# Optimization experiments

Measured on AMD Instinct MI355X. Metric: run time of the kernel, lower is better.

The kernel has to match this reference:

```python
import jax, jax.numpy as jnp
import numpy as np

MAX_TOTAL = 20        # max_total_size
MAX_PER_CLASS = 20    # max_output_size_per_class
SCORE_TH = 0.5        # score_threshold
IOU_TH = 0.5          # tf combined NMS default iou_threshold
K_CAND = 200          # top candidates per class considered for NMS
VARIANCES = jnp.array([0.1, 0.1, 0.2, 0.2], jnp.float32)


def setup_inputs() -> dict:
    key = jax.random.key(0)
    k1, k2, k3, k4, k5, k6 = jax.random.split(key, 6)
    B, N, C = 64, 8732, 21
    pred_deltas = jax.random.normal(k1, (B, N, 4), jnp.float32)
    pred_labels = jax.random.uniform(k2, (B, N, C), dtype=jnp.float32)
    # synthetic normalized anchors (y1,x1,y2,x2) with valid extents
    cy = jax.random.uniform(k3, (N,), dtype=jnp.float32)
    cx = jax.random.uniform(k4, (N,), dtype=jnp.float32)
    h = jax.random.uniform(k5, (N,), dtype=jnp.float32, minval=0.05, maxval=0.3)
    w = jax.random.uniform(k6, (N,), dtype=jnp.float32, minval=0.05, maxval=0.3)
    anchors = jnp.stack([cy - h / 2, cx - w / 2, cy + h / 2, cx + w / 2], axis=-1)
    return {"pred_deltas": pred_deltas, "pred_labels": pred_labels, "anchors": anchors}


def _decode(anchors, deltas):
    # anchors [N,4] (y1,x1,y2,x2); deltas [B,N,4] (dy,dx,dh,dw) -> boxes [B,N,4]
    ah = anchors[:, 2] - anchors[:, 0]
    aw = anchors[:, 3] - anchors[:, 1]
    acy = anchors[:, 0] + 0.5 * ah
    acx = anchors[:, 1] + 0.5 * aw
    cy = deltas[..., 0] * ah + acy
    cx = deltas[..., 1] * aw + acx
    h = jnp.exp(deltas[..., 2]) * ah
    w = jnp.exp(deltas[..., 3]) * aw
    return jnp.stack([cy - 0.5 * h, cx - 0.5 * w, cy + 0.5 * h, cx + 0.5 * w], axis=-1)


def _pairwise_iou(boxes):
    # boxes [K,4] -> iou [K,K]
    y1, x1, y2, x2 = boxes[:, 0], boxes[:, 1], boxes[:, 2], boxes[:, 3]
    area = (y2 - y1) * (x2 - x1)
    ih = jnp.clip(jnp.minimum(y2[:, None], y2[None, :]) - jnp.maximum(y1[:, None], y1[None, :]), 0.0)
    iw = jnp.clip(jnp.minimum(x2[:, None], x2[None, :]) - jnp.maximum(x1[:, None], x1[None, :]), 0.0)
    inter = ih * iw
    return inter / (area[:, None] + area[None, :] - inter + 1e-8)


def _nms_one_class(scores, boxes):
    # scores [N], boxes [N,4] -> (top scores [MAX_PER_CLASS], boxes [MAX_PER_CLASS,4])
    vals, idx = jax.lax.top_k(scores, K_CAND)          # sorted desc
    cboxes = boxes[idx]                                # [K,4]
    iou = _pairwise_iou(cboxes)                        # [K,K]
    valid = vals > SCORE_TH
    ar = jnp.arange(K_CAND)

    def body(i, keep):
        suppressed = jnp.any(keep & (iou[i] > IOU_TH) & (ar < i))
        return keep.at[i].set(valid[i] & ~suppressed)

    keep = jax.lax.fori_loop(0, K_CAND, body, jnp.zeros(K_CAND, dtype=bool))
    kept_scores = jnp.where(keep, vals, 0.0)
    top_vals, top_i = jax.lax.top_k(kept_scores, MAX_PER_CLASS)
    return top_vals, cboxes[top_i]


def reference(pred_deltas, pred_labels, anchors):
    deltas = pred_deltas * VARIANCES                       # variance scaling
    boxes = _decode(anchors, deltas)                       # [B,N,4]
    # zero out all class scores where argmax class == 0 (background)
    lab_map = jnp.argmax(pred_labels, axis=-1, keepdims=True)
    scores = jnp.where(lab_map != 0, pred_labels, 0.0)     # [B,N,C]

    per_class = jax.vmap(_nms_one_class, in_axes=(1, None))   # over classes
    per_batch = jax.vmap(per_class, in_axes=(0, 0))           # over batch
    cls_scores, cls_boxes = per_batch(scores, boxes)          # [B,C,P], [B,C,P,4]

    B, C, P = cls_scores.shape
    flat_scores = cls_scores.reshape(B, C * P)
    flat_boxes = cls_boxes.reshape(B, C * P, 4)
    class_ids = jnp.broadcast_to(jnp.arange(C, dtype=jnp.float32)[:, None], (C, P)).reshape(-1)

    top_vals, top_i = jax.lax.top_k(flat_scores, MAX_TOTAL)   # [B,MAX_TOTAL]
    final_boxes = jnp.take_along_axis(flat_boxes, top_i[..., None], axis=1)
    final_boxes = jnp.clip(final_boxes, 0.0, 1.0)             # combined NMS clip_boxes=True
    valid = top_vals > 0.0
    final_boxes = jnp.where(valid[..., None], final_boxes, 0.0)
    final_labels = jnp.where(valid, class_ids[top_i], 0.0)
    return final_boxes, top_vals, final_labels
```

## Files before the change

### kernel.cpp

```cpp
#include <hip/hip_runtime.h>
#include <stdint.h>

typedef unsigned long long u64;
typedef unsigned int u32;

#define BATCH 64
#define NANCH 8732
#define NF4   2183
#define NCLS 21
#define KCAND 200
#define PPC 20
#define PTOT 20

__global__ __launch_bounds__(256) void kdecode(
    const float* __restrict__ deltas, const float* __restrict__ labels,
    const float* __restrict__ anchors, float* __restrict__ boxes,
    unsigned char* __restrict__ msk, float* __restrict__ scoresT, int useT)
{
#pragma clang fp contract(off)
    int n = blockIdx.x * 256 + threadIdx.x;
    int b = blockIdx.y;
    if (n >= NANCH) return;
    const float* lab = labels + ((size_t)b * NANCH + n) * NCLS;
    float v[NCLS];
#pragma unroll
    for (int c = 0; c < NCLS; ++c) v[c] = lab[c];
    float mx = v[0]; int am = 0;
#pragma unroll
    for (int c = 1; c < NCLS; ++c) if (v[c] > mx) { mx = v[c]; am = c; }
    bool mk = (am != 0);
    msk[(size_t)b * NANCH + n] = mk ? 1 : 0;
    if (useT) {
#pragma unroll
        for (int c = 0; c < NCLS; ++c)
            scoresT[((size_t)b * NCLS + c) * NANCH + n] = mk ? v[c] : 0.0f;
    }
    float4 d = ((const float4*)deltas)[(size_t)b * NANCH + n];
    float4 a = ((const float4*)anchors)[n];
    float ah = a.z - a.x, aw = a.w - a.y;
    float acy = a.x + 0.5f * ah, acx = a.y + 0.5f * aw;
    float cy = (d.x * 0.1f) * ah + acy;
    float cx = (d.y * 0.1f) * aw + acx;
    float hh = expf(d.z * 0.2f) * ah;
    float ww = expf(d.w * 0.2f) * aw;
    float4 o;
    o.x = cy - 0.5f * hh; o.y = cx - 0.5f * ww;
    o.z = cy + 0.5f * hh; o.w = cx + 0.5f * ww;
    ((float4*)boxes)[(size_t)b * NANCH + n] = o;
}

__device__ __forceinline__ u64 shflxor64(u64 x, int m) {
    return (u64)__shfl_xor((long long)x, m, 64);
}

__device__ __forceinline__ void suffixFind(const u32* hist, u32* waveTot, int nb, int need,
                                           int* sSel, int* sAbove, int* sH,
                                           int tid, int lane, int wv)
{
    int K = (nb + 255) >> 8;
    int base = tid * K;
    u32 own = 0;
    for (int q = 0; q < K; ++q) { int bi = base + q; own += (bi < nb) ? hist[bi] : 0u; }
    u32 s = own;
#pragma unroll
    for (int d = 1; d < 64; d <<= 1) {
        u32 o = __shfl_down(s, d, 64);
        if (lane + d < 64) s += o;
    }
    if (lane == 0) waveTot[wv] = s;
    __syncthreads();
    u32 add = 0;
    for (int w = wv + 1; w < 4; ++w) add += waveTot[w];
    u32 cum = (s - own) + add;
    for (int q = K - 1; q >= 0; --q) {
        int bi = base + q;
        u32 hh = (bi < nb) ? hist[bi] : 0u;
        if (cum < (u32)need && cum + hh >= (u32)need) { *sSel = bi; *sAbove = (int)cum; *sH = (int)hh; }
        cum += hh;
    }
    __syncthreads();
}

__global__ __launch_bounds__(256) void knms(
    const float* __restrict__ labels, const unsigned char* __restrict__ msk,
    const float* __restrict__ scoresT, const float* __restrict__ boxes,
    float* __restrict__ clsScores, float* __restrict__ clsBoxes, int useT)
{
#pragma clang fp contract(off)
    __shared__ __align__(16) char smem[8192];
    u32*   hist = (u32*)smem;
    float* cbY1 = (float*)smem;
    float* cbX1 = (float*)(smem + 1024);
    float* cbY2 = (float*)(smem + 2048);
    float* cbX2 = (float*)(smem + 3072);
    float* cbAr = (float*)(smem + 4096);
    float* cVal = (float*)(smem + 5120);
    u64*   iouT = (u64*)(smem + 6144);
    __shared__ u64 candKey[256];
    __shared__ u32 waveTot[4];
    __shared__ float outS[PPC];
    __shared__ float outB[PPC * 4];
    __shared__ int sSel, sAbove, sH, sN, sKP;

    const int tid = threadIdx.x;
    const int lane = tid & 63;
    const int wv = tid >> 6;
    const int bc = blockIdx.x;
    const int b = bc / NCLS;
    const int c = bc % NCLS;

    float4 rs[9];
    if (useT) {
        const float4* src4 = (const float4*)(scoresT + (size_t)bc * NANCH);
#pragma unroll
        for (int q = 0; q < 9; ++q) {
            int i4 = q * 256 + tid;
            rs[q] = (i4 < NF4) ? src4[i4] : make_float4(0.f, 0.f, 0.f, 0.f);
        }
    } else {
#pragma unroll
        for (int q = 0; q < 9; ++q) {
            float vv[4];
#pragma unroll
            for (int e = 0; e < 4; ++e) {
                int n = (q * 256 + tid) * 4 + e;
                float v = 0.f;
                if (n < NANCH && msk[(size_t)b * NANCH + n])
                    v = labels[((size_t)b * NANCH + n) * NCLS + c];
                vv[e] = v;
            }
            rs[q] = make_float4(vv[0], vv[1], vv[2], vv[3]);
        }
    }

    for (int q = tid; q < 2048; q += 256) hist[q] = 0;
    if (tid == 0) { sSel = 0; sAbove = 0; sH = 0; sN = 0; sKP = 0; }
    __syncthreads();
#pragma unroll
    for (int q = 0; q < 9; ++q) {
        if (q * 256 + tid < NF4) {
            float vv[4] = {rs[q].x, rs[q].y, rs[q].z, rs[q].w};
#pragma unroll
            for (int e = 0; e < 4; ++e) {
                u32 t = (u32)(vv[e] * 16777216.0f);
                atomicAdd(&hist[t >> 13], 1u);
            }
        }
    }
    __syncthreads();
    suffixFind(hist, waveTot, 2048, KCAND, &sSel, &sAbove, &sH, tid, lane, wv);
    int A = sAbove, h = sH;
    u32 T = (u32)sSel << 13;
    int cnt = A + h;

    u32 width = 8192;
    for (int level = 0; level < 2 && cnt > 256; ++level) {
        int nb = (level == 0) ? 256 : 32;
        int shift = (level == 0) ? 5 : 0;
        for (int q = tid; q < nb; q += 256) hist[q] = 0;
        if (tid == 0) { sSel = 0; sAbove = 0; sH = 0; }
        __syncthreads();
#pragma unroll
        for (int q = 0; q < 9; ++q) {
            if (q * 256 + tid < NF4) {
                float vv[4] = {rs[q].x, rs[q].y, rs[q].z, rs[q].w};
#pragma unroll
                for (int e = 0; e < 4; ++e) {
                    u32 t = (u32)(vv[e] * 16777216.0f);
                    if (t >= T && t - T < width) atomicAdd(&hist[(t - T) >> shift], 1u);
                }
            }
        }
        __syncthreads();
        suffixFind(hist, waveTot, nb, KCAND - A, &sSel, &sAbove, &sH, tid, lane, wv);
        h = sH;
        A += sAbove;
        T += (u32)sSel << shift;
        cnt = A + h;
        width = 1u << shift;
    }

#pragma unroll
    for (int q = 0; q < 9; ++q) {
        if (q * 256 + tid < NF4) {
            float vv[4] = {rs[q].x, rs[q].y, rs[q].z, rs[q].w};
#pragma unroll
            for (int e = 0; e < 4; ++e) {
                float v = vv[e];
                u32 t = (u32)(v * 16777216.0f);
                if (t >= T) {
                    int slot = atomicAdd(&sN, 1);
                    if (slot < 256) {
                        int n = (q * 256 + tid) * 4 + e;
                        candKey[slot] = ((u64)__float_as_uint(v) << 32) | (u32)(~(u32)n);
                    }
                }
            }
        }
    }
    __syncthreads();
    int nc = sN; if (nc > 256) nc = 256;

    u64 x = (tid < nc) ? candKey[tid] : 0ull;
    for (int k = 2; k <= 256; k <<= 1) {
        for (int j = k >> 1; j > 0; j >>= 1) {
            u64 y;
            if (j < 64) {
                y = shflxor64(x, j);
            } else {
                __syncthreads();
                candKey[tid] = x;
                __syncthreads();
                y = candKey[tid ^ j];
            }
            bool keepMax = ((tid & k) == 0) == ((tid & j) == 0);
            u64 mx = (x > y) ? x : y;
            u64 mn = (x > y) ? y : x;
            x = keepMax ? mx : mn;
        }
    }

    float myV = __uint_as_float((u32)(x >> 32));
    float myY1 = 0.f, myX1 = 0.f, myY2 = 0.f, myX2 = 0.f, myAr = 0.f;
    if (tid < KCAND) {
        u32 idx = ~(u32)x;
        float4 bx = ((const float4*)boxes)[(size_t)b * NANCH + idx];
        myY1 = bx.x; myX1 = bx.y; myY2 = bx.z; myX2 = bx.w;
        myAr = (bx.z - bx.x) * (bx.w - bx.y);
    } else {
        myV = 0.f;
    }
    __syncthreads();
    cbY1[tid] = myY1; cbX1[tid] = myX1; cbY2[tid] = myY2; cbX2[tid] = myX2;
    cbAr[tid] = myAr; cVal[tid] = myV;

    u64 k0 = 0, k1 = 0, k2 = 0, k3 = 0;
    int KPw = 0;
    for (int t0 = 0; t0 < 4; ++t0) {
        __syncthreads();
        if (sKP >= PPC) break;
        int rowBase = t0 * 64;
        int rows = KCAND - rowBase; if (rows > 64) rows = 64;
        for (int r = wv; r < rows; r += 4) {
            int i = rowBase + r;
            float y1i = cbY1[i], x1i = cbX1[i], y2i = cbY2[i], x2i = cbX2[i], ari = cbAr[i];
            for (int cg = 0; cg <= t0; ++cg) {
                int j = cg * 64 + lane;
                float ih = fminf(y2i, cbY2[j]) - fmaxf(y1i, cbY1[j]);
                ih = fmaxf(ih, 0.0f);
                float iw = fminf(x2i, cbX2[j]) - fmaxf(x1i, cbX1[j]);
                iw = fmaxf(iw, 0.0f);
                float inter = ih * iw;
                float iou = inter / (ari + cbAr[j] - inter + 1e-8f);
                u64 bal = __ballot(iou > 0.5f);
                if (lane == 0) iouT[r * 4 + cg] = bal;
            }
        }
        __syncthreads();
        if (tid < 64) {
            int i = rowBase + lane;
            u64 r0 = 0, r1 = 0, r2 = 0, r3 = 0;
            bool vld = false;
            if (lane < rows) {
                r0 = iouT[lane * 4 + 0]; r1 = iouT[lane * 4 + 1];
                r2 = iouT[lane * 4 + 2]; r3 = iouT[lane * 4 + 3];
                vld = cVal[i] > 0.5f;
            }
            for (int l = 0; l < rows; ++l) {
                int mydec = (vld && !((k0 & r0) | (k1 & r1) | (k2 & r2) | (k3 & r3))) ? 1 : 0;
                int d = __shfl(mydec, l, 64);
                if (d) {
                    u64 bit = 1ull << l;
                    if (t0 == 0) k0 |= bit; else if (t0 == 1) k1 |= bit;
                    else if (t0 == 2) k2 |= bit; else k3 |= bit;
                    ++KPw;
                    if (KPw >= PPC) break;
                }
            }
            if (tid == 0) sKP = KPw;
        }
    }
    __syncthreads();

    if (tid < PPC) outS[tid] = 0.0f;
    if (tid < PPC * 4) outB[tid] = 0.0f;
    __syncthreads();

    if (tid < 64) {
        int base = 0;
#pragma unroll
        for (int chunk = 0; chunk < 4; ++chunk) {
            u64 kw = (chunk == 0) ? k0 : (chunk == 1) ? k1 : (chunk == 2) ? k2 : k3;
            int i = chunk * 64 + tid;
            bool kept = ((kw >> tid) & 1ull) != 0;
            int rank = base + (int)__popcll(kw & ((1ull << tid) - 1ull));
            if (kept && rank < PPC && i < KCAND) {
                outS[rank] = cVal[i];
                outB[rank * 4 + 0] = cbY1[i];
                outB[rank * 4 + 1] = cbX1[i];
                outB[rank * 4 + 2] = cbY2[i];
                outB[rank * 4 + 3] = cbX2[i];
            }
            base += (int)__popcll(kw);
        }
    }
    __syncthreads();
    if (tid < PPC) clsScores[(size_t)bc * PPC + tid] = outS[tid];
    if (tid < PPC * 4) clsBoxes[(size_t)bc * PPC * 4 + tid] = outB[tid];
}

__global__ __launch_bounds__(512) void kmerge(
    const float* __restrict__ clsScores, const float* __restrict__ clsBoxes,
    float* __restrict__ out)
{
#pragma clang fp contract(off)
    __shared__ u64 key[512];
    const int tid = threadIdx.x;
    const int b = blockIdx.x;
    const int F = NCLS * PPC;
    u64 kk = 0;
    if (tid < F) {
        float v = clsScores[(size_t)b * F + tid];
        kk = ((u64)__float_as_uint(v) << 32) | (u32)(~(u32)tid);
    }
    key[tid] = kk;
    for (int k = 2; k <= 512; k <<= 1)
        for (int j = k >> 1; j > 0; j >>= 1) {
            __syncthreads();
            int ixj = tid ^ j;
            if (ixj > tid) {
                u64 a = key[tid], bb = key[ixj];
                if (((tid & k) == 0) ? (a < bb) : (a > bb)) { key[tid] = bb; key[ixj] = a; }
            }
        }
    __syncthreads();
    if (tid < PTOT) {
        u64 kx = key[tid];
        float v = __uint_as_float((u32)(kx >> 32));
        u32 f = ~((u32)kx);
        bool valid = (v > 0.0f) && (f < (u32)F);
        float cls = valid ? (float)(f / PPC) : 0.0f;
        float* oB = out;
        float* oV = out + (size_t)BATCH * PTOT * 4;
        float* oL = oV + (size_t)BATCH * PTOT;
#pragma unroll
        for (int q = 0; q < 4; ++q) {
            float xq = 0.0f;
            if (valid) {
                xq = clsBoxes[((size_t)b * F + f) * 4 + q];
                xq = fminf(fmaxf(xq, 0.0f), 1.0f);
            }
            oB[((size_t)b * PTOT + tid) * 4 + q] = xq;
        }
        oV[(size_t)b * PTOT + tid] = v;
        oL[(size_t)b * PTOT + tid] = cls;
    }
}

extern "C" void kernel_launch(void* const* d_in, const int* in_sizes, int n_in,
                              void* d_out, int out_size, void* d_ws, size_t ws_size,
                              hipStream_t stream)
{
    const float* deltas  = (const float*)d_in[0];
    const float* labels  = (const float*)d_in[1];
    const float* anchors = (const float*)d_in[2];
    float* out = (float*)d_out;
    char* ws = (char*)d_ws;

    const size_t boxesOff = 0;
    const size_t maskOff  = 8941568;
    const size_t csOff    = 9500416;
    const size_t cbOff    = 9607936;
    const size_t stOff    = 10038016;
    const size_t needT    = 56981248;

    float* boxes = (float*)(ws + boxesOff);
    unsigned char* msk = (unsigned char*)(ws + maskOff);
    float* clsScores = (float*)(ws + csOff);
    float* clsBoxes  = (float*)(ws + cbOff);
    float* scoresT   = (float*)(ws + stOff);
    int useT = (ws_size >= needT) ? 1 : 0;
    if (!useT) scoresT = boxes;

    dim3 gA((NANCH + 255) / 256, BATCH);
    kdecode<<<gA, 256, 0, stream>>>(deltas, labels, anchors, boxes, msk, scoresT, useT);
    knms<<<BATCH * NCLS, 256, 0, stream>>>(labels, msk, scoresT, boxes, clsScores, clsBoxes, useT);
    kmerge<<<BATCH, 512, 0, stream>>>(clsScores, clsBoxes, out);
}
```

Baseline: 70.77 us.

## Store transposed scores as 16-bit keys and decode boxes only for candidates

The transposed per-class score buffer is now written as 16-bit fixed-point keys padded to a multiple of 8 anchors, which halves the bytes written by kdecode and read by knms. Scores below 0.5 are skipped in the histogram, and a shorter two-stage radix select picks the threshold. The exact float score is re-read from labels only for the surviving candidates. Box decoding moves out of kdecode into knms and runs only for the top 200 candidates per class, so the full boxes buffer is no longer written or read. The cost is extra scattered reads of labels, deltas and anchors inside knms. Candidates that tie under 16-bit quantization may also overflow the 256-slot buffer.

```diff
diff --git a/kernel.cpp b/kernel.cpp
--- a/kernel.cpp
+++ b/kernel.cpp
@@ -3,24 +3,33 @@
 
 typedef unsigned long long u64;
 typedef unsigned int u32;
+typedef unsigned short u16;
 
 #define BATCH 64
 #define NANCH 8732
-#define NF4   2183
+#define NPAD  8736
+#define NCHUNK 1092
 #define NCLS 21
 #define KCAND 200
 #define PPC 20
 #define PTOT 20
 
 __global__ __launch_bounds__(256) void kdecode(
-    const float* __restrict__ deltas, const float* __restrict__ labels,
-    const float* __restrict__ anchors, float* __restrict__ boxes,
-    unsigned char* __restrict__ msk, float* __restrict__ scoresT, int useT)
+    const float* __restrict__ labels,
+    unsigned char* __restrict__ msk, u16* __restrict__ st16, int useT)
 {
 #pragma clang fp contract(off)
     int n = blockIdx.x * 256 + threadIdx.x;
     int b = blockIdx.y;
-    if (n >= NANCH) return;
+    if (n >= NPAD) return;
+    if (n >= NANCH) {
+        if (useT) {
+#pragma unroll
+            for (int c = 0; c < NCLS; ++c)
+                st16[((size_t)b * NCLS + c) * NPAD + n] = 0;
+        }
+        return;
+    }
     const float* lab = labels + ((size_t)b * NANCH + n) * NCLS;
     float v[NCLS];
 #pragma unroll
@@ -32,21 +41,11 @@
     msk[(size_t)b * NANCH + n] = mk ? 1 : 0;
     if (useT) {
 #pragma unroll
-        for (int c = 0; c < NCLS; ++c)
-            scoresT[((size_t)b * NCLS + c) * NANCH + n] = mk ? v[c] : 0.0f;
-    }
-    float4 d = ((const float4*)deltas)[(size_t)b * NANCH + n];
-    float4 a = ((const float4*)anchors)[n];
-    float ah = a.z - a.x, aw = a.w - a.y;
-    float acy = a.x + 0.5f * ah, acx = a.y + 0.5f * aw;
-    float cy = (d.x * 0.1f) * ah + acy;
-    float cx = (d.y * 0.1f) * aw + acx;
-    float hh = expf(d.z * 0.2f) * ah;
-    float ww = expf(d.w * 0.2f) * aw;
-    float4 o;
-    o.x = cy - 0.5f * hh; o.y = cx - 0.5f * ww;
-    o.z = cy + 0.5f * hh; o.w = cx + 0.5f * ww;
-    ((float4*)boxes)[(size_t)b * NANCH + n] = o;
+        for (int c = 0; c < NCLS; ++c) {
+            u16 t = mk ? (u16)(u32)(v[c] * 65536.0f) : (u16)0;
+            st16[((size_t)b * NCLS + c) * NPAD + n] = t;
+        }
+    }
 }
 
 __device__ __forceinline__ u64 shflxor64(u64 x, int m) {
@@ -54,7 +53,7 @@
 }
 
 __device__ __forceinline__ void suffixFind(const u32* hist, u32* waveTot, int nb, int need,
-                                           int* sSel, int* sAbove, int* sH,
+                                           int* sSel, int* sAbove, int* sH, int* sTot,
                                            int tid, int lane, int wv)
 {
     int K = (nb + 255) >> 8;
@@ -69,6 +68,7 @@
     }
     if (lane == 0) waveTot[wv] = s;
     __syncthreads();
+    if (tid == 0 && sTot) *sTot = (int)(waveTot[0] + waveTot[1] + waveTot[2] + waveTot[3]);
     u32 add = 0;
     for (int w = wv + 1; w < 4; ++w) add += waveTot[w];
     u32 cum = (s - own) + add;
@@ -83,7 +83,8 @@
 
 __global__ __launch_bounds__(256) void knms(
     const float* __restrict__ labels, const unsigned char* __restrict__ msk,
-    const float* __restrict__ scoresT, const float* __restrict__ boxes,
+    const u16* __restrict__ st16,
+    const float* __restrict__ deltas, const float* __restrict__ anchors,
     float* __restrict__ clsScores, float* __restrict__ clsBoxes, int useT)
 {
 #pragma clang fp contract(off)
@@ -100,7 +101,7 @@
     __shared__ u32 waveTot[4];
     __shared__ float outS[PPC];
     __shared__ float outB[PPC * 4];
-    __shared__ int sSel, sAbove, sH, sN, sKP;
+    __shared__ int sSel, sAbove, sH, sTot, sN, sKP;
 
     const int tid = threadIdx.x;
     const int lane = tid & 63;
@@ -109,90 +110,95 @@
     const int b = bc / NCLS;
     const int c = bc % NCLS;
 
-    float4 rs[9];
+    uint4 rc[5];
     if (useT) {
-        const float4* src4 = (const float4*)(scoresT + (size_t)bc * NANCH);
-#pragma unroll
-        for (int q = 0; q < 9; ++q) {
+        const uint4* src = (const uint4*)(st16 + (size_t)bc * NPAD);
+#pragma unroll
+        for (int q = 0; q < 5; ++q) {
             int i4 = q * 256 + tid;
-            rs[q] = (i4 < NF4) ? src4[i4] : make_float4(0.f, 0.f, 0.f, 0.f);
+            rc[q] = (i4 < NCHUNK) ? src[i4] : make_uint4(0, 0, 0, 0);
         }
     } else {
-#pragma unroll
-        for (int q = 0; q < 9; ++q) {
-            float vv[4];
-#pragma unroll
-            for (int e = 0; e < 4; ++e) {
-                int n = (q * 256 + tid) * 4 + e;
-                float v = 0.f;
-                if (n < NANCH && msk[(size_t)b * NANCH + n])
-                    v = labels[((size_t)b * NANCH + n) * NCLS + c];
-                vv[e] = v;
-            }
-            rs[q] = make_float4(vv[0], vv[1], vv[2], vv[3]);
-        }
-    }
-
-    for (int q = tid; q < 2048; q += 256) hist[q] = 0;
-    if (tid == 0) { sSel = 0; sAbove = 0; sH = 0; sN = 0; sKP = 0; }
-    __syncthreads();
-#pragma unroll
-    for (int q = 0; q < 9; ++q) {
-        if (q * 256 + tid < NF4) {
-            float vv[4] = {rs[q].x, rs[q].y, rs[q].z, rs[q].w};
-#pragma unroll
-            for (int e = 0; e < 4; ++e) {
-                u32 t = (u32)(vv[e] * 16777216.0f);
-                atomicAdd(&hist[t >> 13], 1u);
-            }
-        }
-    }
-    __syncthreads();
-    suffixFind(hist, waveTot, 2048, KCAND, &sSel, &sAbove, &sH, tid, lane, wv);
-    int A = sAbove, h = sH;
-    u32 T = (u32)sSel << 13;
-    int cnt = A + h;
-
-    u32 width = 8192;
-    for (int level = 0; level < 2 && cnt > 256; ++level) {
-        int nb = (level == 0) ? 256 : 32;
-        int shift = (level == 0) ? 5 : 0;
-        for (int q = tid; q < nb; q += 256) hist[q] = 0;
-        if (tid == 0) { sSel = 0; sAbove = 0; sH = 0; }
+        for (int q = 0; q < 5; ++q) {
+            int chunk = q * 256 + tid;
+            u32 w4[4] = {0, 0, 0, 0};
+            if (chunk < NCHUNK) {
+                for (int w = 0; w < 4; ++w)
+                    for (int h = 0; h < 2; ++h) {
+                        int n = chunk * 8 + w * 2 + h;
+                        u32 t = 0;
+                        if (n < NANCH && msk[(size_t)b * NANCH + n]) {
+                            float v = labels[((size_t)b * NANCH + n) * NCLS + c];
+                            t = (u32)(v * 65536.0f);
+                        }
+                        w4[w] |= t << (16 * h);
+                    }
+            }
+            rc[q] = make_uint4(w4[0], w4[1], w4[2], w4[3]);
+        }
+    }
+
+    for (int q = tid; q < 1024; q += 256) hist[1024 + q] = 0;
+    if (tid == 0) { sSel = -1; sAbove = 0; sH = 0; sTot = 0; sN = 0; sKP = 0; }
+    __syncthreads();
+#pragma unroll
+    for (int q = 0; q < 5; ++q) {
+        if (q * 256 + tid < NCHUNK) {
+            u32 w4[4] = {rc[q].x, rc[q].y, rc[q].z, rc[q].w};
+#pragma unroll
+            for (int w = 0; w < 4; ++w) {
+                u32 lo = w4[w] & 0xFFFFu, hi = w4[w] >> 16;
+                if (lo & 0x8000u) atomicAdd(&hist[lo >> 5], 1u);
+                if (hi & 0x8000u) atomicAdd(&hist[hi >> 5], 1u);
+            }
+        }
+    }
+    __syncthreads();
+    suffixFind(hist + 1024, waveTot, 1024, KCAND, &sSel, &sAbove, &sH, &sTot, tid, lane, wv);
+
+    int A, cnt; u32 T16;
+    if (sTot < KCAND) { T16 = 32768u; A = 0; cnt = sTot; }
+    else { A = sAbove; T16 = (u32)(1024 + sSel) << 5; cnt = A + sH; }
+
+    if (cnt > 256) {
+        if (tid < 32) hist[tid] = 0;
+        if (tid == 0) { sSel = -1; sAbove = 0; sH = 0; }
         __syncthreads();
 #pragma unroll
-        for (int q = 0; q < 9; ++q) {
-            if (q * 256 + tid < NF4) {
-                float vv[4] = {rs[q].x, rs[q].y, rs[q].z, rs[q].w};
-#pragma unroll
-                for (int e = 0; e < 4; ++e) {
-                    u32 t = (u32)(vv[e] * 16777216.0f);
-                    if (t >= T && t - T < width) atomicAdd(&hist[(t - T) >> shift], 1u);
+        for (int q = 0; q < 5; ++q) {
+            if (q * 256 + tid < NCHUNK) {
+                u32 w4[4] = {rc[q].x, rc[q].y, rc[q].z, rc[q].w};
+#pragma unroll
+                for (int w = 0; w < 4; ++w) {
+                    u32 lo = w4[w] & 0xFFFFu, hi = w4[w] >> 16;
+                    if (lo >= T16 && lo < T16 + 32) atomicAdd(&hist[lo - T16], 1u);
+                    if (hi >= T16 && hi < T16 + 32) atomicAdd(&hist[hi - T16], 1u);
                 }
             }
         }
         __syncthreads();
-        suffixFind(hist, waveTot, nb, KCAND - A, &sSel, &sAbove, &sH, tid, lane, wv);
-        h = sH;
+        suffixFind(hist, waveTot, 32, KCAND - A, &sSel, &sAbove, &sH, nullptr, tid, lane, wv);
         A += sAbove;
-        T += (u32)sSel << shift;
-        cnt = A + h;
-        width = 1u << shift;
-    }
-
-#pragma unroll
-    for (int q = 0; q < 9; ++q) {
-        if (q * 256 + tid < NF4) {
-            float vv[4] = {rs[q].x, rs[q].y, rs[q].z, rs[q].w};
-#pragma unroll
-            for (int e = 0; e < 4; ++e) {
-                float v = vv[e];
-                u32 t = (u32)(v * 16777216.0f);
-                if (t >= T) {
-                    int slot = atomicAdd(&sN, 1);
-                    if (slot < 256) {
-                        int n = (q * 256 + tid) * 4 + e;
-                        candKey[slot] = ((u64)__float_as_uint(v) << 32) | (u32)(~(u32)n);
+        T16 += (u32)sSel;
+        cnt = A + sH;
+    }
+
+#pragma unroll
+    for (int q = 0; q < 5; ++q) {
+        int chunk = q * 256 + tid;
+        if (chunk < NCHUNK) {
+            u32 w4[4] = {rc[q].x, rc[q].y, rc[q].z, rc[q].w};
+#pragma unroll
+            for (int w = 0; w < 4; ++w) {
+#pragma unroll
+                for (int h = 0; h < 2; ++h) {
+                    u32 t = (h == 0) ? (w4[w] & 0xFFFFu) : (w4[w] >> 16);
+                    if (t >= T16) {
+                        int n = chunk * 8 + w * 2 + h;
+                        float v = labels[((size_t)b * NANCH + n) * NCLS + c];
+                        int slot = atomicAdd(&sN, 1);
+                        if (slot < 256)
+                            candKey[slot] = ((u64)__float_as_uint(v) << 32) | (u32)(~(u32)n);
                     }
                 }
             }
@@ -222,11 +228,19 @@
 
     float myV = __uint_as_float((u32)(x >> 32));
     float myY1 = 0.f, myX1 = 0.f, myY2 = 0.f, myX2 = 0.f, myAr = 0.f;
-    if (tid < KCAND) {
-        u32 idx = ~(u32)x;
-        float4 bx = ((const float4*)boxes)[(size_t)b * NANCH + idx];
-        myY1 = bx.x; myX1 = bx.y; myY2 = bx.z; myX2 = bx.w;
-        myAr = (bx.z - bx.x) * (bx.w - bx.y);
+    u32 idx = ~(u32)x;
+    if (tid < KCAND && idx < (u32)NANCH) {
+        float4 d = ((const float4*)deltas)[(size_t)b * NANCH + idx];
+        float4 a = ((const float4*)anchors)[idx];
+        float ah = a.z - a.x, aw = a.w - a.y;
+        float acy = a.x + 0.5f * ah, acx = a.y + 0.5f * aw;
+        float cy = (d.x * 0.1f) * ah + acy;
+        float cx = (d.y * 0.1f) * aw + acx;
+        float hh2 = expf(d.z * 0.2f) * ah;
+        float ww2 = expf(d.w * 0.2f) * aw;
+        myY1 = cy - 0.5f * hh2; myX1 = cx - 0.5f * ww2;
+        myY2 = cy + 0.5f * hh2; myX2 = cx + 0.5f * ww2;
+        myAr = (myY2 - myY1) * (myX2 - myX1);
     } else {
         myV = 0.f;
     }
@@ -367,23 +381,21 @@
     float* out = (float*)d_out;
     char* ws = (char*)d_ws;
 
-    const size_t boxesOff = 0;
-    const size_t maskOff  = 8941568;
-    const size_t csOff    = 9500416;
-    const size_t cbOff    = 9607936;
-    const size_t stOff    = 10038016;
-    const size_t needT    = 56981248;
-
-    float* boxes = (float*)(ws + boxesOff);
-    unsigned char* msk = (unsigned char*)(ws + maskOff);
+    const size_t mskOff = 0;
+    const size_t csOff  = 558848;
+    const size_t cbOff  = 666368;
+    const size_t stOff  = 1096448;
+    const size_t needT  = 24578816;
+
+    unsigned char* msk = (unsigned char*)(ws + mskOff);
     float* clsScores = (float*)(ws + csOff);
     float* clsBoxes  = (float*)(ws + cbOff);
-    float* scoresT   = (float*)(ws + stOff);
+    u16* st16        = (u16*)(ws + stOff);
     int useT = (ws_size >= needT) ? 1 : 0;
-    if (!useT) scoresT = boxes;
-
-    dim3 gA((NANCH + 255) / 256, BATCH);
-    kdecode<<<gA, 256, 0, stream>>>(deltas, labels, anchors, boxes, msk, scoresT, useT);
-    knms<<<BATCH * NCLS, 256, 0, stream>>>(labels, msk, scoresT, boxes, clsScores, clsBoxes, useT);
+
+    dim3 gA((NPAD + 255) / 256, BATCH);
+    kdecode<<<gA, 256, 0, stream>>>(labels, msk, st16, useT);
+    knms<<<BATCH * NCLS, 256, 0, stream>>>(labels, msk, st16, deltas, anchors,
+                                           clsScores, clsBoxes, useT);
     kmerge<<<BATCH, 512, 0, stream>>>(clsScores, clsBoxes, out);
 }
```

New measurement: 57.95 us. -18.1%, faster.
